# Performance work log

Hardware: AMD Instinct MI355X
Metric: run time of the kernel (lower is better)

## Reference

```python
import jax, jax.numpy as jnp
import numpy as np
import math

B, N = 1, 512
C_S, C_Z, C_H, H, PQ, PV = 384, 128, 16, 12, 4, 8
INF, EPS = 100000.0, 1e-8


def setup_inputs() -> dict:
    key = jax.random.key(0)
    ks = jax.random.split(key, 16)
    sc = 0.02
    return {
        "s": jax.random.normal(ks[0], (B, N, C_S), jnp.float32),
        "z": jax.random.normal(ks[1], (B, N, N, C_Z), jnp.float32),
        "t_trans": jax.random.normal(ks[2], (B, N, 3), jnp.float32),
        "t_rots": jax.random.normal(ks[3], (B, N, 3, 3), jnp.float32),
        "mask": jnp.ones((B, N), jnp.float32),
        "Wq": jax.random.normal(ks[4], (C_S, H * C_H), jnp.float32) * sc,
        "bq": jnp.zeros((H * C_H,), jnp.float32),
        "Wkv": jax.random.normal(ks[5], (C_S, 2 * H * C_H), jnp.float32) * sc,
        "bkv": jnp.zeros((2 * H * C_H,), jnp.float32),
        "Wqp": jax.random.normal(ks[6], (C_S, H * PQ * 3), jnp.float32) * sc,
        "bqp": jnp.zeros((H * PQ * 3,), jnp.float32),
        "Wkvp": jax.random.normal(ks[7], (C_S, H * (PQ + PV) * 3), jnp.float32) * sc,
        "bkvp": jnp.zeros((H * (PQ + PV) * 3,), jnp.float32),
        "Wb": jax.random.normal(ks[8], (C_Z, H), jnp.float32) * sc,
        "bb": jnp.zeros((H,), jnp.float32),
        "head_weights": jnp.full((H,), 0.5413, jnp.float32),  # softplus^-1(1) init
        "Wout": jax.random.normal(ks[9], (H * (C_Z + C_H + PV * 4), C_S), jnp.float32) * sc,
        "bout": jnp.zeros((C_S,), jnp.float32),
    }


def _split3_stack(x):
    # torch.split into 3 chunks along -1, then stack on new last axis -> [..., P, 3]
    return jnp.stack(jnp.split(x, 3, axis=-1), axis=-1)


def reference(s, z, t_trans, t_rots, mask, Wq, bq, Wkv, bkv, Wqp, bqp, Wkvp, bkvp,
              Wb, bb, head_weights, Wout, bout):
    q = (s @ Wq + bq).reshape(B, N, H, C_H)
    kv = (s @ Wkv + bkv).reshape(B, N, H, 2 * C_H)
    k, v = kv[..., :C_H], kv[..., C_H:]

    # point projections, moved to global frame: r @ p + t
    qp = _split3_stack(s @ Wqp + bqp)                      # [B,N,H*PQ,3] local
    qp = jnp.einsum('bnij,bnpj->bnpi', t_rots, qp) + t_trans[:, :, None, :]
    q_pts = qp.reshape(B, N, H, PQ, 3)
    kvp = _split3_stack(s @ Wkvp + bkvp)                   # [B,N,H*(PQ+PV),3]
    kvp = jnp.einsum('bnij,bnpj->bnpi', t_rots, kvp) + t_trans[:, :, None, :]
    kvp = kvp.reshape(B, N, H, PQ + PV, 3)
    k_pts, v_pts = kvp[..., :PQ, :], kvp[..., PQ:, :]

    b = z @ Wb + bb                                        # [B,N,N,H]

    a = jnp.einsum('bihc,bjhc->bhij', q, k) * math.sqrt(1.0 / (3 * C_H))
    a = a + math.sqrt(1.0 / 3) * jnp.transpose(b, (0, 3, 1, 2))

    # point-distance attention: [B,N,N,H,PQ]
    d2 = jnp.sum((q_pts[:, :, None] - k_pts[:, None]) ** 2, axis=-1)
    hw = jax.nn.softplus(head_weights) * math.sqrt(1.0 / (3 * (PQ * 9.0 / 2)))
    a = a + (-0.5) * jnp.einsum('bijhp,h->bhij', d2, hw)

    square_mask = INF * (mask[:, :, None] * mask[:, None, :] - 1.0)  # [B,N,N]
    a = jax.nn.softmax(a + square_mask[:, None], axis=-1)  # [B,H,N,N]

    o = jnp.einsum('bhij,bjhc->bihc', a, v).reshape(B, N, H * C_H)

    o_pt = jnp.einsum('bhij,bjhpx->bihpx', a, v_pts)       # [B,N,H,PV,3] global
    # invert frame: r^T @ (p - t)
    o_pt = jnp.einsum('bnji,bnhpj->bnhpi', t_rots, o_pt - t_trans[:, :, None, None, :])
    o_pt_norm = jnp.sqrt(jnp.sum(o_pt ** 2, axis=-1) + EPS).reshape(B, N, H * PV)
    o_pt = o_pt.reshape(B, N, H * PV, 3)

    o_pair = jnp.einsum('bhij,bijc->bihc', a, z).reshape(B, N, H * C_Z)

    cat = jnp.concatenate(
        [o, o_pt[..., 0], o_pt[..., 1], o_pt[..., 2], o_pt_norm, o_pair], axis=-1)
    return cat @ Wout + bout
```

## Files before the change

### kernel.cpp

```cpp
#include <hip/hip_runtime.h>
#include <math.h>

#define N 512
#define CS 384
#define CZ 128
#define CH 16
#define NH 12
#define PQ 4
#define PV 8

#define OFF_Q     0
#define OFF_K     98304
#define OFF_V     196608
#define OFF_QRAW  294912
#define OFF_KVRAW 368640
#define OFF_QPTS  589824
#define OFF_KPTS  663552
#define OFF_VPTS  737280
#define OFF_A     884736
#define OFF_CAT   4030464

__global__ __launch_bounds__(256) void proj_kernel(
    const float* __restrict__ s,
    const float* __restrict__ Wq,  const float* __restrict__ bq,
    const float* __restrict__ Wkv, const float* __restrict__ bkv,
    const float* __restrict__ Wqp, const float* __restrict__ bqp,
    const float* __restrict__ Wkvp,const float* __restrict__ bkvp,
    float* __restrict__ ws)
{
    __shared__ float st[16 * CS];
    const int n0 = blockIdx.x * 16;
    for (int idx = threadIdx.x * 4; idx < 16 * CS; idx += 256 * 4)
        *(float4*)&st[idx] = *(const float4*)&s[n0 * CS + idx];
    __syncthreads();

    const int tc = threadIdx.x & 15;
    const int tr = threadIdx.x >> 4;
    const int u0 = blockIdx.y * 64 + tc * 4;

    const float* W; const float* bptr; int ncol, lc0;
    if (u0 < 192)      { W = Wq;   bptr = bq;   ncol = 192; lc0 = u0; }
    else if (u0 < 576) { W = Wkv;  bptr = bkv;  ncol = 384; lc0 = u0 - 192; }
    else if (u0 < 720) { W = Wqp;  bptr = bqp;  ncol = 144; lc0 = u0 - 576; }
    else               { W = Wkvp; bptr = bkvp; ncol = 432; lc0 = u0 - 720; }

    float acc[4] = {0.f, 0.f, 0.f, 0.f};

    #pragma unroll 2
    for (int k = 0; k < CS; k += 4) {
        float4 w0 = *(const float4*)&W[(k + 0) * ncol + lc0];
        float4 w1 = *(const float4*)&W[(k + 1) * ncol + lc0];
        float4 w2 = *(const float4*)&W[(k + 2) * ncol + lc0];
        float4 w3 = *(const float4*)&W[(k + 3) * ncol + lc0];
        float4 sv = *(const float4*)&st[tr * CS + k];
        acc[0] += sv.x * w0.x + sv.y * w1.x + sv.z * w2.x + sv.w * w3.x;
        acc[1] += sv.x * w0.y + sv.y * w1.y + sv.z * w2.y + sv.w * w3.y;
        acc[2] += sv.x * w0.z + sv.y * w1.z + sv.z * w2.z + sv.w * w3.z;
        acc[3] += sv.x * w0.w + sv.y * w1.w + sv.z * w2.w + sv.w * w3.w;
    }

    const int n = n0 + tr;
    #pragma unroll
    for (int c = 0; c < 4; c++) {
        const int u = u0 + c;
        const float bias = bptr[lc0 + c];
        int oidx;
        if (u < 192) oidx = OFF_Q + n * 192 + u;
        else if (u < 576) {
            int lc = u - 192, h = lc >> 5, w = lc & 31;
            oidx = (w < 16) ? OFF_K + n * 192 + h * 16 + w
                            : OFF_V + n * 192 + h * 16 + (w - 16);
        } else if (u < 720) oidx = OFF_QRAW + n * 144 + (u - 576);
        else                oidx = OFF_KVRAW + n * 432 + (u - 720);
        ws[oidx] = acc[c] + bias;
    }
}

__global__ __launch_bounds__(192) void point_kernel(
    const float* __restrict__ t_trans, const float* __restrict__ t_rots,
    float* __restrict__ ws)
{
    const int n = blockIdx.x;
    const int t = threadIdx.x;
    __shared__ float R[9], tr[3];
    if (t < 9) R[t] = t_rots[n * 9 + t];
    if (t < 3) tr[t] = t_trans[n * 3 + t];
    __syncthreads();

    float x0, x1, x2;
    int base;
    if (t < 48) {
        int idx = t;
        x0 = ws[OFF_QRAW + n * 144 + 0 * 48 + idx];
        x1 = ws[OFF_QRAW + n * 144 + 1 * 48 + idx];
        x2 = ws[OFF_QRAW + n * 144 + 2 * 48 + idx];
        int h = idx >> 2, p = idx & 3;
        base = OFF_QPTS + ((n * NH + h) * PQ + p) * 3;
    } else {
        int idx = t - 48;
        x0 = ws[OFF_KVRAW + n * 432 + 0 * 144 + idx];
        x1 = ws[OFF_KVRAW + n * 432 + 1 * 144 + idx];
        x2 = ws[OFF_KVRAW + n * 432 + 2 * 144 + idx];
        int h = idx / 12, p = idx % 12;
        if (p < PQ) base = OFF_KPTS + ((n * NH + h) * PQ + p) * 3;
        else        base = OFF_VPTS + (n * NH * PV + h * PV + (p - PQ)) * 3;
    }
    ws[base + 0] = R[0] * x0 + R[1] * x1 + R[2] * x2 + tr[0];
    ws[base + 1] = R[3] * x0 + R[4] * x1 + R[5] * x2 + tr[1];
    ws[base + 2] = R[6] * x0 + R[7] * x1 + R[8] * x2 + tr[2];
}

__global__ __launch_bounds__(192) void logitA_kernel(
    const float* __restrict__ mask, const float* __restrict__ hweights,
    float* __restrict__ ws)
{
    const int j0 = blockIdx.x * 16;
    const int i0 = blockIdx.y * 16;
    const int t = threadIdx.x;

    __shared__ float qt[16 * 200];
    __shared__ float kt[16 * 200];
    __shared__ float qpt[16 * 148];
    __shared__ float kpt[16 * 148];
    __shared__ float mi[16], mj[16];

    {
        const float* src = ws + OFF_Q + i0 * 192;
        for (int idx = t * 4; idx < 3072; idx += 768) {
            float4 v = *(const float4*)&src[idx];
            *(float4*)&qt[(idx / 192) * 200 + idx % 192] = v;
        }
    }
    {
        const float* src = ws + OFF_K + j0 * 192;
        for (int idx = t * 4; idx < 3072; idx += 768) {
            float4 v = *(const float4*)&src[idx];
            *(float4*)&kt[(idx / 192) * 200 + idx % 192] = v;
        }
    }
    {
        const float* src = ws + OFF_QPTS + i0 * 144;
        for (int idx = t * 4; idx < 2304; idx += 768) {
            float4 v = *(const float4*)&src[idx];
            *(float4*)&qpt[(idx / 144) * 148 + idx % 144] = v;
        }
    }
    {
        const float* src = ws + OFF_KPTS + j0 * 144;
        for (int idx = t * 4; idx < 2304; idx += 768) {
            float4 v = *(const float4*)&src[idx];
            *(float4*)&kpt[(idx / 144) * 148 + idx % 144] = v;
        }
    }
    if (t < 16) { mi[t] = mask[i0 + t]; mj[t] = mask[j0 + t]; }
    __syncthreads();

    const int jj = t & 15;
    const int h = t >> 4;
    const float hw = log1pf(expf(hweights[h])) * 0.13608276348795434f;
    const float cqk = 0.14433756729740643f;

    float4 kr0 = *(const float4*)&kt[jj * 200 + h * 16 + 0];
    float4 kr1 = *(const float4*)&kt[jj * 200 + h * 16 + 4];
    float4 kr2 = *(const float4*)&kt[jj * 200 + h * 16 + 8];
    float4 kr3 = *(const float4*)&kt[jj * 200 + h * 16 + 12];
    float4 kp0 = *(const float4*)&kpt[jj * 148 + h * 12 + 0];
    float4 kp1 = *(const float4*)&kpt[jj * 148 + h * 12 + 4];
    float4 kp2 = *(const float4*)&kpt[jj * 148 + h * 12 + 8];
    const float mjv = mj[jj];

    for (int ii = 0; ii < 16; ii++) {
        float4 q0 = *(const float4*)&qt[ii * 200 + h * 16 + 0];
        float4 q1 = *(const float4*)&qt[ii * 200 + h * 16 + 4];
        float4 q2 = *(const float4*)&qt[ii * 200 + h * 16 + 8];
        float4 q3 = *(const float4*)&qt[ii * 200 + h * 16 + 12];
        float qk = q0.x * kr0.x + q0.y * kr0.y + q0.z * kr0.z + q0.w * kr0.w
                 + q1.x * kr1.x + q1.y * kr1.y + q1.z * kr1.z + q1.w * kr1.w
                 + q2.x * kr2.x + q2.y * kr2.y + q2.z * kr2.z + q2.w * kr2.w
                 + q3.x * kr3.x + q3.y * kr3.y + q3.z * kr3.z + q3.w * kr3.w;
        float4 p0 = *(const float4*)&qpt[ii * 148 + h * 12 + 0];
        float4 p1 = *(const float4*)&qpt[ii * 148 + h * 12 + 4];
        float4 p2 = *(const float4*)&qpt[ii * 148 + h * 12 + 8];
        float e, d2 = 0.f;
        e = p0.x - kp0.x; d2 += e * e;  e = p0.y - kp0.y; d2 += e * e;
        e = p0.z - kp0.z; d2 += e * e;  e = p0.w - kp0.w; d2 += e * e;
        e = p1.x - kp1.x; d2 += e * e;  e = p1.y - kp1.y; d2 += e * e;
        e = p1.z - kp1.z; d2 += e * e;  e = p1.w - kp1.w; d2 += e * e;
        e = p2.x - kp2.x; d2 += e * e;  e = p2.y - kp2.y; d2 += e * e;
        e = p2.z - kp2.z; d2 += e * e;  e = p2.w - kp2.w; d2 += e * e;
        float sm = 100000.0f * (mi[ii] * mjv - 1.0f);
        ws[OFF_A + ((size_t)(i0 + ii) * NH + h) * N + j0 + jj] =
            qk * cqk - 0.5f * hw * d2 + sm;
    }
}

__global__ __launch_bounds__(512) void bsoft_kernel(
    const float* __restrict__ z, const float* __restrict__ Wb,
    const float* __restrict__ bb, float* __restrict__ ws)
{
    const int i = blockIdx.x;
    const int t = threadIdx.x;
    __shared__ float zt[128 * 132];
    __shared__ float wbt[12 * 132];
    __shared__ float wred[8][4];

    for (int idx = t; idx < CZ * NH; idx += 512) {
        int c = idx / NH, h = idx % NH;
        wbt[h * 132 + c] = Wb[idx];
    }

    const int jj = t & 127;
    const int hg = t >> 7;
    const int h0 = hg * 3;
    const float bb0 = bb[h0], bb1 = bb[h0 + 1], bb2 = bb[h0 + 2];
    const float cb = 0.5773502691896258f;

    float lg[3][4];

    for (int T = 0; T < 4; T++) {
        __syncthreads();
        const float* zsrc = z + ((size_t)i * N + T * 128) * CZ;
        for (int idx = t * 4; idx < 16384; idx += 2048) {
            float4 v = *(const float4*)&zsrc[idx];
            *(float4*)&zt[(idx >> 7) * 132 + (idx & 127)] = v;
        }
        __syncthreads();

        float a0 = bb0, a1 = bb1, a2 = bb2;
        const float* zr = &zt[jj * 132];
        const float* w0 = &wbt[(h0 + 0) * 132];
        const float* w1 = &wbt[(h0 + 1) * 132];
        const float* w2 = &wbt[(h0 + 2) * 132];
        #pragma unroll
        for (int c = 0; c < CZ; c += 4) {
            float4 zq = *(const float4*)&zr[c];
            float4 q0 = *(const float4*)&w0[c];
            float4 q1 = *(const float4*)&w1[c];
            float4 q2 = *(const float4*)&w2[c];
            a0 += zq.x * q0.x + zq.y * q0.y + zq.z * q0.z + zq.w * q0.w;
            a1 += zq.x * q1.x + zq.y * q1.y + zq.z * q1.z + zq.w * q1.w;
            a2 += zq.x * q2.x + zq.y * q2.y + zq.z * q2.z + zq.w * q2.w;
        }
        const float* arow = ws + OFF_A + (size_t)i * NH * N + T * 128 + jj;
        lg[0][T] = arow[(size_t)(h0 + 0) * N] + cb * a0;
        lg[1][T] = arow[(size_t)(h0 + 1) * N] + cb * a1;
        lg[2][T] = arow[(size_t)(h0 + 2) * N] + cb * a2;
    }

    const int wv = t >> 6;
    float mx[3], sm[3];
    #pragma unroll
    for (int r = 0; r < 3; r++) {
        float m = fmaxf(fmaxf(lg[r][0], lg[r][1]), fmaxf(lg[r][2], lg[r][3]));
        #pragma unroll
        for (int o = 32; o > 0; o >>= 1) m = fmaxf(m, __shfl_xor(m, o));
        mx[r] = m;
    }
    if ((t & 63) == 0) {
        wred[wv][0] = mx[0]; wred[wv][1] = mx[1]; wred[wv][2] = mx[2];
    }
    __syncthreads();
    #pragma unroll
    for (int r = 0; r < 3; r++)
        mx[r] = fmaxf(wred[hg * 2][r], wred[hg * 2 + 1][r]);
    __syncthreads();
    #pragma unroll
    for (int r = 0; r < 3; r++) {
        float s = 0.f;
        #pragma unroll
        for (int T = 0; T < 4; T++) { lg[r][T] = __expf(lg[r][T] - mx[r]); s += lg[r][T]; }
        #pragma unroll
        for (int o = 32; o > 0; o >>= 1) s += __shfl_xor(s, o);
        sm[r] = s;
    }
    if ((t & 63) == 0) {
        wred[wv][0] = sm[0]; wred[wv][1] = sm[1]; wred[wv][2] = sm[2];
    }
    __syncthreads();
    #pragma unroll
    for (int r = 0; r < 3; r++) {
        float inv = 1.0f / (wred[hg * 2][r] + wred[hg * 2 + 1][r]);
        float* prow = ws + OFF_A + ((size_t)i * NH + h0 + r) * N + jj;
        #pragma unroll
        for (int T = 0; T < 4; T++)
            prow[T * 128] = lg[r][T] * inv;
    }
}

__global__ __launch_bounds__(960) void finish_kernel(
    const float* __restrict__ z, const float* __restrict__ t_trans,
    const float* __restrict__ t_rots, const float* __restrict__ ws_c,
    float* __restrict__ ws)
{
    const int i = blockIdx.x;
    const int t = threadIdx.x;
    __shared__ float a_s[12 * 520];
    __shared__ float pr_pair[192 * 8];
    __shared__ float pr_o[192];
    __shared__ float pr_pt[96 * 3];

    {
        const float* src = ws_c + OFF_A + (size_t)i * (NH * N);
        for (int idx = t * 4; idx < NH * N; idx += 960 * 4) {
            float4 v = *(const float4*)&src[idx];
            int h = idx >> 9, j = idx & 511;
            *(float4*)&a_s[h * 520 + j] = v;
        }
    }
    __syncthreads();

    float* cat = ws + OFF_CAT + (size_t)i * 2112;

    float4 accA = {0,0,0,0}, accB = {0,0,0,0};
    float accO = 0.f;
    float g0 = 0.f, g1 = 0.f, g2 = 0.f;

    int jh = 0, v = 0;

    if (t < 384) {
        jh = (t >= 192); v = t - jh * 192;
        const int cg = v & 31;
        const int hs = v >> 5;
        const float* zb = z + (size_t)i * N * CZ + cg * 4;
        const float* ahA = a_s + hs * 520;
        const float* ahB = a_s + (hs + 6) * 520;
        const int j0 = jh * 256;
        for (int jo = 0; jo < 256; jo += 8) {
            const int j = j0 + jo;
            float4 z0 = *(const float4*)&zb[(size_t)(j + 0) * CZ];
            float4 z1 = *(const float4*)&zb[(size_t)(j + 1) * CZ];
            float4 z2 = *(const float4*)&zb[(size_t)(j + 2) * CZ];
            float4 z3 = *(const float4*)&zb[(size_t)(j + 3) * CZ];
            float4 z4 = *(const float4*)&zb[(size_t)(j + 4) * CZ];
            float4 z5 = *(const float4*)&zb[(size_t)(j + 5) * CZ];
            float4 z6 = *(const float4*)&zb[(size_t)(j + 6) * CZ];
            float4 z7 = *(const float4*)&zb[(size_t)(j + 7) * CZ];
            float4 aA0 = *(const float4*)&ahA[j];
            float4 aA1 = *(const float4*)&ahA[j + 4];
            float4 aB0 = *(const float4*)&ahB[j];
            float4 aB1 = *(const float4*)&ahB[j + 4];
            accA.x += aA0.x * z0.x + aA0.y * z1.x + aA0.z * z2.x + aA0.w * z3.x
                    + aA1.x * z4.x + aA1.y * z5.x + aA1.z * z6.x + aA1.w * z7.x;
            accA.y += aA0.x * z0.y + aA0.y * z1.y + aA0.z * z2.y + aA0.w * z3.y
                    + aA1.x * z4.y + aA1.y * z5.y + aA1.z * z6.y + aA1.w * z7.y;
            accA.z += aA0.x * z0.z + aA0.y * z1.z + aA0.z * z2.z + aA0.w * z3.z
                    + aA1.x * z4.z + aA1.y * z5.z + aA1.z * z6.z + aA1.w * z7.z;
            accA.w += aA0.x * z0.w + aA0.y * z1.w + aA0.z * z2.w + aA0.w * z3.w
                    + aA1.x * z4.w + aA1.y * z5.w + aA1.z * z6.w + aA1.w * z7.w;
            accB.x += aB0.x * z0.x + aB0.y * z1.x + aB0.z * z2.x + aB0.w * z3.x
                    + aB1.x * z4.x + aB1.y * z5.x + aB1.z * z6.x + aB1.w * z7.x;
            accB.y += aB0.x * z0.y + aB0.y * z1.y + aB0.z * z2.y + aB0.w * z3.y
                    + aB1.x * z4.y + aB1.y * z5.y + aB1.z * z6.y + aB1.w * z7.y;
            accB.z += aB0.x * z0.z + aB0.y * z1.z + aB0.z * z2.z + aB0.w * z3.z
                    + aB1.x * z4.z + aB1.y * z5.z + aB1.z * z6.z + aB1.w * z7.z;
            accB.w += aB0.x * z0.w + aB0.y * z1.w + aB0.z * z2.w + aB0.w * z3.w
                    + aB1.x * z4.w + aB1.y * z5.w + aB1.z * z6.w + aB1.w * z7.w;
        }
    } else if (t < 768) {
        const int u = t - 384;
        jh = (u >= 192); v = u - jh * 192;
        const int h = v >> 4, cc = v & 15;
        const float* vcol = ws_c + OFF_V + h * 16 + cc;
        const float* ah = a_s + h * 520;
        const int j0 = jh * 256;
        for (int jo = 0; jo < 256; jo += 8) {
            const int j = j0 + jo;
            float v0 = vcol[(j + 0) * 192];
            float v1 = vcol[(j + 1) * 192];
            float v2 = vcol[(j + 2) * 192];
            float v3 = vcol[(j + 3) * 192];
            float v4 = vcol[(j + 4) * 192];
            float v5 = vcol[(j + 5) * 192];
            float v6 = vcol[(j + 6) * 192];
            float v7 = vcol[(j + 7) * 192];
            float4 a0 = *(const float4*)&ah[j];
            float4 a1 = *(const float4*)&ah[j + 4];
            accO += a0.x * v0 + a0.y * v1 + a0.z * v2 + a0.w * v3
                  + a1.x * v4 + a1.y * v5 + a1.z * v6 + a1.w * v7;
        }
    } else {
        const int u = t - 768;
        jh = (u >= 96); v = u - jh * 96;
        const int h = v >> 3, p = v & 7;
        const float* vp = ws_c + OFF_VPTS + (h * PV + p) * 3;
        const float* ah = a_s + h * 520;
        const int j0 = jh * 256;
        for (int jo = 0; jo < 256; jo += 4) {
            const int j = j0 + jo;
            const float* p0 = vp + (size_t)(j + 0) * 288;
            const float* p1 = vp + (size_t)(j + 1) * 288;
            const float* p2 = vp + (size_t)(j + 2) * 288;
            const float* p3 = vp + (size_t)(j + 3) * 288;
            float x0 = p0[0], y0 = p0[1], w0 = p0[2];
            float x1 = p1[0], y1 = p1[1], w1 = p1[2];
            float x2 = p2[0], y2 = p2[1], w2 = p2[2];
            float x3 = p3[0], y3 = p3[1], w3 = p3[2];
            float4 a4 = *(const float4*)&ah[j];
            g0 += a4.x * x0 + a4.y * x1 + a4.z * x2 + a4.w * x3;
            g1 += a4.x * y0 + a4.y * y1 + a4.z * y2 + a4.w * y3;
            g2 += a4.x * w0 + a4.y * w1 + a4.z * w2 + a4.w * w3;
        }
    }

    if (jh == 1) {
        if (t < 384) {
            float* d = pr_pair + v * 8;
            d[0] = accA.x; d[1] = accA.y; d[2] = accA.z; d[3] = accA.w;
            d[4] = accB.x; d[5] = accB.y; d[6] = accB.z; d[7] = accB.w;
        } else if (t < 768) {
            pr_o[v] = accO;
        } else {
            pr_pt[v * 3 + 0] = g0; pr_pt[v * 3 + 1] = g1; pr_pt[v * 3 + 2] = g2;
        }
    }
    __syncthreads();

    if (jh == 0) {
        if (t < 384) {
            const float* d = pr_pair + v * 8;
            accA.x += d[0]; accA.y += d[1]; accA.z += d[2]; accA.w += d[3];
            accB.x += d[4]; accB.y += d[5]; accB.z += d[6]; accB.w += d[7];
            const int cg = v & 31, hs = v >> 5;
            *(float4*)&cat[576 + hs * CZ + cg * 4]       = accA;
            *(float4*)&cat[576 + (hs + 6) * CZ + cg * 4] = accB;
        } else if (t < 768) {
            accO += pr_o[v];
            const int h = v >> 4, cc = v & 15;
            cat[h * 16 + cc] = accO;
        } else {
            g0 += pr_pt[v * 3 + 0]; g1 += pr_pt[v * 3 + 1]; g2 += pr_pt[v * 3 + 2];
            float R[9], ti[3];
            #pragma unroll
            for (int x = 0; x < 9; x++) R[x] = t_rots[i * 9 + x];
            #pragma unroll
            for (int x = 0; x < 3; x++) ti[x] = t_trans[i * 3 + x];
            g0 -= ti[0]; g1 -= ti[1]; g2 -= ti[2];
            float l0 = R[0] * g0 + R[3] * g1 + R[6] * g2;
            float l1 = R[1] * g0 + R[4] * g1 + R[7] * g2;
            float l2 = R[2] * g0 + R[5] * g1 + R[8] * g2;
            float nrm = sqrtf(l0 * l0 + l1 * l1 + l2 * l2 + 1e-8f);
            const int h = v >> 3, p = v & 7;
            int e = h * PV + p;
            cat[192 + e] = l0;
            cat[288 + e] = l1;
            cat[384 + e] = l2;
            cat[480 + e] = nrm;
        }
    }
}

__global__ __launch_bounds__(384, 4) void out_kernel(
    const float* __restrict__ Wout, const float* __restrict__ ws_c,
    float* __restrict__ ws)
{
    const int rt = blockIdx.x;
    const int kc = blockIdx.y;
    const int t = threadIdx.x;
    __shared__ float ct[16 * 132];
    for (int idx = t * 4; idx < 16 * 132; idx += 384 * 4) {
        int rr = idx / 132, kk = idx % 132;
        *(float4*)&ct[idx] =
            *(const float4*)&ws_c[OFF_CAT + (size_t)(rt * 16 + rr) * 2112 + kc * 132 + kk];
    }
    __syncthreads();
    const int cq = t % 96, rg = t / 96;
    const int c0 = cq * 4;
    float acc[4][4] = {};
    const float* Wp = Wout + (size_t)kc * 132 * 384 + c0;
    #pragma unroll 4
    for (int kk = 0; kk < 132; kk += 4) {
        float4 w0 = *(const float4*)&Wp[(size_t)(kk + 0) * 384];
        float4 w1 = *(const float4*)&Wp[(size_t)(kk + 1) * 384];
        float4 w2 = *(const float4*)&Wp[(size_t)(kk + 2) * 384];
        float4 w3 = *(const float4*)&Wp[(size_t)(kk + 3) * 384];
        #pragma unroll
        for (int r = 0; r < 4; r++) {
            float4 sv = *(const float4*)&ct[(rg * 4 + r) * 132 + kk];
            acc[r][0] += sv.x * w0.x + sv.y * w1.x + sv.z * w2.x + sv.w * w3.x;
            acc[r][1] += sv.x * w0.y + sv.y * w1.y + sv.z * w2.y + sv.w * w3.y;
            acc[r][2] += sv.x * w0.z + sv.y * w1.z + sv.z * w2.z + sv.w * w3.z;
            acc[r][3] += sv.x * w0.w + sv.y * w1.w + sv.z * w2.w + sv.w * w3.w;
        }
    }
    float* dst = ws + OFF_A + (size_t)kc * (512 * 384);
    #pragma unroll
    for (int r = 0; r < 4; r++) {
        float4 a4 = make_float4(acc[r][0], acc[r][1], acc[r][2], acc[r][3]);
        *(float4*)&dst[(size_t)(rt * 16 + rg * 4 + r) * 384 + c0] = a4;
    }
}

__global__ __launch_bounds__(256) void reduce_out_kernel(
    const float* __restrict__ bout, const float* __restrict__ ws,
    float* __restrict__ out)
{
    const int idx = (blockIdx.x * 256 + threadIdx.x) * 4;
    const int col = idx % 384;
    float4 acc = *(const float4*)&bout[col];
    #pragma unroll
    for (int kc = 0; kc < 16; kc++) {
        float4 p = *(const float4*)&ws[OFF_A + (size_t)kc * (512 * 384) + idx];
        acc.x += p.x; acc.y += p.y; acc.z += p.z; acc.w += p.w;
    }
    *(float4*)&out[idx] = acc;
}

extern "C" void kernel_launch(void* const* d_in, const int* in_sizes, int n_in,
                              void* d_out, int out_size, void* d_ws, size_t ws_size,
                              hipStream_t stream) {
    const float* s       = (const float*)d_in[0];
    const float* z       = (const float*)d_in[1];
    const float* t_trans = (const float*)d_in[2];
    const float* t_rots  = (const float*)d_in[3];
    const float* mask    = (const float*)d_in[4];
    const float* Wq      = (const float*)d_in[5];
    const float* bq      = (const float*)d_in[6];
    const float* Wkv     = (const float*)d_in[7];
    const float* bkv     = (const float*)d_in[8];
    const float* Wqp     = (const float*)d_in[9];
    const float* bqp     = (const float*)d_in[10];
    const float* Wkvp    = (const float*)d_in[11];
    const float* bkvp    = (const float*)d_in[12];
    const float* Wb      = (const float*)d_in[13];
    const float* bb      = (const float*)d_in[14];
    const float* hweights= (const float*)d_in[15];
    const float* Wout    = (const float*)d_in[16];
    const float* bout    = (const float*)d_in[17];
    float* ws  = (float*)d_ws;
    float* out = (float*)d_out;

    proj_kernel<<<dim3(32, 18), 256, 0, stream>>>(s, Wq, bq, Wkv, bkv, Wqp, bqp, Wkvp, bkvp, ws);
    point_kernel<<<512, 192, 0, stream>>>(t_trans, t_rots, ws);
    logitA_kernel<<<dim3(32, 32), 192, 0, stream>>>(mask, hweights, ws);
    bsoft_kernel<<<512, 512, 0, stream>>>(z, Wb, bb, ws);
    finish_kernel<<<512, 960, 0, stream>>>(z, t_trans, t_rots, ws, ws);
    out_kernel<<<dim3(32, 16), 384, 0, stream>>>(Wout, ws, ws);
    reduce_out_kernel<<<192, 256, 0, stream>>>(bout, ws, out);
}
```

Baseline: 374.8 us.

## Compute pair-bias softmax with 128 threads, each handling 4 columns per tile

```diff
diff --git a/kernel.cpp b/kernel.cpp
--- a/kernel.cpp
+++ b/kernel.cpp
@@ -194,7 +194,7 @@
     }
 }
 
-__global__ __launch_bounds__(512) void bsoft_kernel(
+__global__ __launch_bounds__(512, 4) void bsoft_kernel(
     const float* __restrict__ z, const float* __restrict__ Wb,
     const float* __restrict__ bb, float* __restrict__ ws)
 {
@@ -202,20 +202,19 @@
     const int t = threadIdx.x;
     __shared__ float zt[128 * 132];
     __shared__ float wbt[12 * 132];
-    __shared__ float wred[8][4];
 
     for (int idx = t; idx < CZ * NH; idx += 512) {
         int c = idx / NH, h = idx % NH;
         wbt[h * 132 + c] = Wb[idx];
     }
 
-    const int jj = t & 127;
-    const int hg = t >> 7;
+    const int jq = t & 31;
+    const int hg = (t >> 5) & 3;
     const int h0 = hg * 3;
     const float bb0 = bb[h0], bb1 = bb[h0 + 1], bb2 = bb[h0 + 2];
     const float cb = 0.5773502691896258f;
 
-    float lg[3][4];
+    float lg[3][4][4];
 
     for (int T = 0; T < 4; T++) {
         __syncthreads();
@@ -226,64 +225,68 @@
         }
         __syncthreads();
 
-        float a0 = bb0, a1 = bb1, a2 = bb2;
-        const float* zr = &zt[jj * 132];
-        const float* w0 = &wbt[(h0 + 0) * 132];
-        const float* w1 = &wbt[(h0 + 1) * 132];
-        const float* w2 = &wbt[(h0 + 2) * 132];
+        if (t < 128) {
+            float a[3][4];
+            #pragma unroll
+            for (int r = 0; r < 3; r++)
+                #pragma unroll
+                for (int k = 0; k < 4; k++) a[r][k] = 0.f;
+            const float* w0 = &wbt[(h0 + 0) * 132];
+            const float* w1 = &wbt[(h0 + 1) * 132];
+            const float* w2 = &wbt[(h0 + 2) * 132];
+            #pragma unroll 4
+            for (int c = 0; c < CZ; c += 4) {
+                float4 q0 = *(const float4*)&w0[c];
+                float4 q1 = *(const float4*)&w1[c];
+                float4 q2 = *(const float4*)&w2[c];
+                #pragma unroll
+                for (int k = 0; k < 4; k++) {
+                    float4 zq = *(const float4*)&zt[(jq + 32 * k) * 132 + c];
+                    a[0][k] += zq.x * q0.x + zq.y * q0.y + zq.z * q0.z + zq.w * q0.w;
+                    a[1][k] += zq.x * q1.x + zq.y * q1.y + zq.z * q1.z + zq.w * q1.w;
+                    a[2][k] += zq.x * q2.x + zq.y * q2.y + zq.z * q2.z + zq.w * q2.w;
+                }
+            }
+            const float* arow = ws + OFF_A + (size_t)i * NH * N + T * 128 + jq;
+            #pragma unroll
+            for (int r = 0; r < 3; r++) {
+                const float* ar = arow + (size_t)(h0 + r) * N;
+                const float bbr = (r == 0) ? bb0 : ((r == 1) ? bb1 : bb2);
+                #pragma unroll
+                for (int k = 0; k < 4; k++)
+                    lg[r][k][T] = ar[32 * k] + cb * (a[r][k] + bbr);
+            }
+        }
+    }
+
+    if (t < 128) {
         #pragma unroll
-        for (int c = 0; c < CZ; c += 4) {
-            float4 zq = *(const float4*)&zr[c];
-            float4 q0 = *(const float4*)&w0[c];
-            float4 q1 = *(const float4*)&w1[c];
-            float4 q2 = *(const float4*)&w2[c];
-            a0 += zq.x * q0.x + zq.y * q0.y + zq.z * q0.z + zq.w * q0.w;
-            a1 += zq.x * q1.x + zq.y * q1.y + zq.z * q1.z + zq.w * q1.w;
-            a2 += zq.x * q2.x + zq.y * q2.y + zq.z * q2.z + zq.w * q2.w;
-        }
-        const float* arow = ws + OFF_A + (size_t)i * NH * N + T * 128 + jj;
-        lg[0][T] = arow[(size_t)(h0 + 0) * N] + cb * a0;
-        lg[1][T] = arow[(size_t)(h0 + 1) * N] + cb * a1;
-        lg[2][T] = arow[(size_t)(h0 + 2) * N] + cb * a2;
-    }
-
-    const int wv = t >> 6;
-    float mx[3], sm[3];
-    #pragma unroll
-    for (int r = 0; r < 3; r++) {
-        float m = fmaxf(fmaxf(lg[r][0], lg[r][1]), fmaxf(lg[r][2], lg[r][3]));
-        #pragma unroll
-        for (int o = 32; o > 0; o >>= 1) m = fmaxf(m, __shfl_xor(m, o));
-        mx[r] = m;
-    }
-    if ((t & 63) == 0) {
-        wred[wv][0] = mx[0]; wred[wv][1] = mx[1]; wred[wv][2] = mx[2];
-    }
-    __syncthreads();
-    #pragma unroll
-    for (int r = 0; r < 3; r++)
-        mx[r] = fmaxf(wred[hg * 2][r], wred[hg * 2 + 1][r]);
-    __syncthreads();
-    #pragma unroll
-    for (int r = 0; r < 3; r++) {
-        float s = 0.f;
-        #pragma unroll
-        for (int T = 0; T < 4; T++) { lg[r][T] = __expf(lg[r][T] - mx[r]); s += lg[r][T]; }
-        #pragma unroll
-        for (int o = 32; o > 0; o >>= 1) s += __shfl_xor(s, o);
-        sm[r] = s;
-    }
-    if ((t & 63) == 0) {
-        wred[wv][0] = sm[0]; wred[wv][1] = sm[1]; wred[wv][2] = sm[2];
-    }
-    __syncthreads();
-    #pragma unroll
-    for (int r = 0; r < 3; r++) {
-        float inv = 1.0f / (wred[hg * 2][r] + wred[hg * 2 + 1][r]);
-        float* prow = ws + OFF_A + ((size_t)i * NH + h0 + r) * N + jj;
-        #pragma unroll
-        for (int T = 0; T < 4; T++)
-            prow[T * 128] = lg[r][T] * inv;
+        for (int r = 0; r < 3; r++) {
+            float m = -1e30f;
+            #pragma unroll
+            for (int k = 0; k < 4; k++)
+                #pragma unroll
+                for (int T = 0; T < 4; T++) m = fmaxf(m, lg[r][k][T]);
+            #pragma unroll
+            for (int o = 16; o > 0; o >>= 1) m = fmaxf(m, __shfl_xor(m, o));
+            float s = 0.f;
+            #pragma unroll
+            for (int k = 0; k < 4; k++)
+                #pragma unroll
+                for (int T = 0; T < 4; T++) {
+                    lg[r][k][T] = __expf(lg[r][k][T] - m);
+                    s += lg[r][k][T];
+                }
+            #pragma unroll
+            for (int o = 16; o > 0; o >>= 1) s += __shfl_xor(s, o);
+            const float inv = 1.0f / s;
+            float* prow = ws + OFF_A + ((size_t)i * NH + h0 + r) * N + jq;
+            #pragma unroll
+            for (int T = 0; T < 4; T++)
+                #pragma unroll
+                for (int k = 0; k < 4; k++)
+                    prow[T * 128 + 32 * k] = lg[r][k][T] * inv;
+        }
     }
 }
 
```

Result: no change. 381.4 us (+1.8%).
